# Kernel optimization log

Hardware: AMD Instinct MI355X
Metric: run time of the kernel (lower is better)

Reference implementation:

```python
import jax, jax.numpy as jnp
import numpy as np

H = 400      # LSTM hidden units
K = 10       # attention window mixture components (mixtures=30 -> alpha/beta/kappa of size K)
V = 61       # vocab_size
NOUT = 121   # MDN head: 1 eos + 20*(pi, mu1, mu2, sigma1, sigma2, rho)


def setup_inputs():
    key = jax.random.key(0)
    ks = jax.random.split(key, 12)
    B, T, U = 32, 600, 64
    s = 0.05
    d = {}
    d['strokes'] = jax.random.normal(ks[0], (B, T, 3), jnp.float32)
    d['sentence'] = jax.random.uniform(ks[1], (B, U, V), dtype=jnp.float32)
    d['W1'] = jax.random.normal(ks[2], (3 + V, 4 * H), jnp.float32) * s
    d['U1r'] = jax.random.normal(ks[3], (H, 4 * H), jnp.float32) * s
    d['b1'] = jnp.zeros((4 * H,), jnp.float32)
    d['Ww'] = jax.random.normal(ks[4], (H, 3 * K), jnp.float32) * s
    d['bw'] = jnp.zeros((3 * K,), jnp.float32)
    d['W2'] = jax.random.normal(ks[5], (3 + V + H, 4 * H), jnp.float32) * s
    d['U2r'] = jax.random.normal(ks[6], (H, 4 * H), jnp.float32) * s
    d['b2'] = jnp.zeros((4 * H,), jnp.float32)
    d['W3'] = jax.random.normal(ks[7], (3 + V + H, 4 * H), jnp.float32) * s
    d['U3r'] = jax.random.normal(ks[8], (H, 4 * H), jnp.float32) * s
    d['b3'] = jnp.zeros((4 * H,), jnp.float32)
    d['Wm'] = jax.random.normal(ks[9], (3 * H, NOUT), jnp.float32) * s
    d['bm'] = jnp.zeros((NOUT,), jnp.float32)
    return d


def _lstm(x_tbd, W, Ur, b, h0, c0):
    # standard Keras-order (i, f, g, o) LSTM over time-major input [T,B,D]
    def step(carry, xt):
        h, c = carry
        z = xt @ W + h @ Ur + b
        i, f, g, o = jnp.split(z, 4, axis=-1)
        c = jax.nn.sigmoid(f) * c + jax.nn.sigmoid(i) * jnp.tanh(g)
        h = jax.nn.sigmoid(o) * jnp.tanh(c)
        return (h, c), h
    _, hs = jax.lax.scan(step, (h0, c0), x_tbd)
    return hs


def _forward(strokes, sentence, W1, U1r, b1, Ww, bw, W2, U2r, b2, W3, U3r, b3, Wm, bm):
    B, T, _ = strokes.shape
    U = sentence.shape[1]
    u_grid = jnp.arange(U, dtype=strokes.dtype)           # character positions
    x_tb = jnp.transpose(strokes, (1, 0, 2))               # [T,B,3]
    h0 = jnp.zeros((B, H), strokes.dtype)
    w0 = jnp.zeros((B, V), strokes.dtype)
    k0 = jnp.zeros((B, K), strokes.dtype)

    def step1(carry, xt):
        # Graves synthesis windowed LSTM cell: LSTM on [x_t, w_{t-1}],
        # then Gaussian-mixture soft attention over the sentence.
        h, c, w, kappa = carry
        xin = jnp.concatenate([xt, w], axis=-1)            # [B, 3+V]
        z = xin @ W1 + h @ U1r + b1
        i, f, g, o = jnp.split(z, 4, axis=-1)
        c = jax.nn.sigmoid(f) * c + jax.nn.sigmoid(i) * jnp.tanh(g)
        h = jax.nn.sigmoid(o) * jnp.tanh(c)
        p = h @ Ww + bw                                    # [B, 3K]
        alpha = jnp.exp(p[:, :K])
        beta = jnp.exp(p[:, K:2 * K])
        kappa = kappa + jnp.exp(p[:, 2 * K:])
        # phi(u) = sum_k alpha_k exp(-beta_k (kappa_k - u)^2)  -> [B,U]
        phi = jnp.einsum('bk,bku->bu', alpha,
                         jnp.exp(-beta[:, :, None] * (kappa[:, :, None] - u_grid) ** 2))
        w = jnp.einsum('bu,buv->bv', phi, sentence)        # soft window [B,V]
        return (h, c, w, kappa), jnp.concatenate([h, w], axis=-1)

    _, o1 = jax.lax.scan(step1, (h0, h0, w0, k0), x_tb)    # [T,B,H+V]
    lstm1 = o1[:, :, :H]
    win = o1[:, :, H:]
    in2 = jnp.concatenate([x_tb, win, lstm1], axis=-1)     # skip1: [T,B,3+V+H]
    lstm2 = _lstm(in2, W2, U2r, b2, h0, h0)
    in3 = jnp.concatenate([x_tb, win, lstm2], axis=-1)     # skip2
    lstm3 = _lstm(in3, W3, U3r, b3, h0, h0)
    y = jnp.concatenate([lstm1, lstm2, lstm3], axis=-1) @ Wm + bm  # [T,B,121]
    # MDN mixture coefficients
    e = jax.nn.sigmoid(y[..., 0:1])
    pi = jax.nn.softmax(y[..., 1:21], axis=-1)
    mu1 = y[..., 21:41]
    mu2 = y[..., 41:61]
    s1 = jnp.exp(y[..., 61:81])
    s2 = jnp.exp(y[..., 81:101])
    rho = jnp.tanh(y[..., 101:121])
    out = jnp.concatenate([e, pi, mu1, mu2, s1, s2, rho], axis=-1)
    return jnp.transpose(out, (1, 0, 2))                   # [B,T,121]


def reference(strokes, sentence, W1, U1r, b1, Ww, bw, W2, U2r, b2, W3, U3r, b3, Wm, bm):
    return _forward(strokes, sentence, W1, U1r, b1, Ww, bw, W2, U2r, b2, W3, U3r, b3, Wm, bm)
```

## Files before the change

kernel.cpp:

```cpp
#include <hip/hip_runtime.h>
#include <math.h>

#define T 600
#define NBLK 235

#define FL1 256
#define FL2 768
#define FL3 1280
#define FLB 1792
#define SH1 2304
#define SH2 2880
#define SH3 3520

#define OFF_UT1 8192
#define SZ_UT1 (1600*480)
#define OFF_UT2 (OFF_UT1 + SZ_UT1)
#define SZ_UT2 (1600*960)
#define OFF_UT3 (OFF_UT2 + SZ_UT2)
#define OFF_WWT (OFF_UT3 + SZ_UT2)
#define SZ_WWT (30*400)
#define OFF_H1 (OFF_WWT + SZ_WWT)
#define SZ_H (600*32*400)
#define OFF_H2 (OFF_H1 + SZ_H)
#define OFF_H3 (OFF_H2 + SZ_H)
#define OFF_W  (OFF_H3 + SZ_H)
#define SZ_W (600*32*61)

#define LDS_W    0
#define LDS_V    19280
#define LDS_Z    34640
#define LDS_C    35408
#define LDS_TOT  35600

__device__ __forceinline__ float sigm(float x) { return 1.f/(1.f+expf(-x)); }

__global__ void init_ws(unsigned* uws) {
    for (int i = threadIdx.x + blockIdx.x*blockDim.x; i < 8192; i += blockDim.x*gridDim.x)
        uws[i] = 0u;
}

__global__ void build_ut(float* __restrict__ ws,
                         const float* __restrict__ W1, const float* __restrict__ U1r,
                         const float* __restrict__ W2, const float* __restrict__ U2r,
                         const float* __restrict__ W3, const float* __restrict__ U3r,
                         const float* __restrict__ Ww) {
    const long N1 = 1600L*480, N2 = 1600L*960;
    const long total = N1 + 2*N2 + 30L*400;
    for (long i = blockIdx.x*(long)blockDim.x + threadIdx.x; i < total;
         i += (long)gridDim.x*blockDim.x) {
        if (i < N1) {
            long c = i / 480, k = i % 480;
            float v = 0.f;
            if (k < 64) v = W1[k*1600 + c];
            else if (k < 464) v = U1r[(k-64)*1600 + c];
            ws[OFF_UT1 + c*480 + k] = v;
        } else if (i < N1 + N2) {
            long ii = i - N1; long c = ii/960, k = ii%960;
            float v = 0.f;
            if (k < 464) v = W2[k*1600 + c];
            else if (k >= 480 && k < 880) v = U2r[(k-480)*1600 + c];
            ws[OFF_UT2 + c*960 + k] = v;
        } else if (i < N1 + 2*N2) {
            long ii = i - N1 - N2; long c = ii/960, k = ii%960;
            float v = 0.f;
            if (k < 464) v = W3[k*1600 + c];
            else if (k >= 480 && k < 880) v = U3r[(k-480)*1600 + c];
            ws[OFF_UT3 + c*960 + k] = v;
        } else {
            long ii = i - N1 - 2*N2; long n = ii/400, k = ii%400;
            ws[OFF_WWT + n*400 + k] = Ww[k*30 + n];
        }
    }
}

__device__ __forceinline__ unsigned ld_cohere(const unsigned* p) {
    unsigned v;
    asm volatile("global_load_dword %0, %1, off sc0 sc1\n\t"
                 "s_waitcnt vmcnt(0)"
                 : "=v"(v) : "v"(p) : "memory");
    return v;
}
__device__ __forceinline__ void st_wt(float* p, float v) {
    asm volatile("global_store_dword %0, %1, off sc0 sc1\n\t"
                 "s_waitcnt vmcnt(0)"
                 :: "v"(p), "v"(v) : "memory");
}
__device__ __forceinline__ void publish(unsigned* flags, unsigned v) {
    #pragma unroll
    for (int r = 0; r < 8; ++r)
        asm volatile("global_store_dword %0, %1, off sc0 sc1"
                     :: "v"(flags + r*64), "v"(v) : "memory");
    asm volatile("s_waitcnt vmcnt(0)" ::: "memory");
}
__device__ __forceinline__ void wait_flag(const unsigned* p, unsigned tgt) {
    int it = 0;
    while (ld_cohere(p) < tgt) {
        if (it > 32) __builtin_amdgcn_s_sleep(2);
        ++it;
    }
}
__device__ __forceinline__ void arrive2(unsigned* shard, unsigned gsize,
                                        unsigned* master, unsigned n,
                                        unsigned* flags, unsigned ep1) {
    unsigned old = __hip_atomic_fetch_add(shard, 1u, __ATOMIC_RELAXED,
                                          __HIP_MEMORY_SCOPE_AGENT);
    if (old + 1u == gsize * ep1) {
        unsigned o2 = __hip_atomic_fetch_add(master, gsize, __ATOMIC_RELAXED,
                                             __HIP_MEMORY_SCOPE_AGENT);
        if (o2 + gsize == n * ep1) publish(flags, ep1);
    }
}
__device__ __forceinline__ void arrive1(unsigned* master, unsigned n,
                                        unsigned* flags, unsigned ep1) {
    unsigned old = __hip_atomic_fetch_add(master, 1u, __ATOMIC_RELAXED,
                                          __HIP_MEMORY_SCOPE_AGENT);
    if (old + 1u == n * ep1) publish(flags, ep1);
}

template<int NQ, int KCN, int K4S, int LO, int HI>
__device__ __forceinline__ void gemm_pass(const float4* __restrict__ w4,
                                          const float4* __restrict__ v4,
                                          int lc0, int kc, int bq, int kofs4,
                                          float acc[8][4]) {
    #pragma unroll
    for (int q = 0; q < NQ; ++q) {
        int kfv = q*KCN + kc;
        if (kfv >= LO && kfv < HI) {
            int xv = kfv ^ ((kfv >> 3) & 7);
            int kfw = kofs4 + kfv;
            int xw = kfw ^ ((kfw >> 3) & 7);
            float4 va[8];
            #pragma unroll
            for (int i = 0; i < 8; ++i) va[i] = v4[(bq*8+i)*120 + xv];
            #pragma unroll
            for (int j = 0; j < 4; ++j) {
                float4 u = w4[(lc0+j)*K4S + xw];
                #pragma unroll
                for (int i = 0; i < 8; ++i)
                    acc[i][j] += va[i].x*u.x + va[i].y*u.y + va[i].z*u.z + va[i].w*u.w;
            }
        }
    }
}

__launch_bounds__(512)
__global__ void hw_main(float* __restrict__ ws,
                        const float* __restrict__ strokes, const float* __restrict__ sentence,
                        const float* __restrict__ b1, const float* __restrict__ b2,
                        const float* __restrict__ b3, const float* __restrict__ bw) {
    extern __shared__ float S[];
    const int tid = threadIdx.x;
    const int bid = blockIdx.x;
    unsigned* uws = (unsigned*)ws;
    unsigned* root1 = uws + 0;
    unsigned* root2 = uws + 64;
    unsigned* root3 = uws + 128;
    unsigned* rootB = uws + 192;
    const int rep = (bid & 7) * 64;
    const unsigned* fl1r = uws + FL1 + rep;
    const unsigned* fl2r = uws + FL2 + rep;
    const unsigned* flBr = uws + FLB + rep;

    int role, unit0 = 0, nu = 0, L = 0, b0a = 0;
    const float* utp = nullptr; const float* biasp = nullptr; float* hout = nullptr;
    if (bid < 67)       { role = 0; L = bid;      unit0 = L*6; nu = (bid==66)?4:6; utp = ws+OFF_UT1; biasp = b1; hout = ws+OFF_H1; }
    else if (bid < 147) { role = 1; L = bid-67;   unit0 = L*5; nu = 5;             utp = ws+OFF_UT2; biasp = b2; hout = ws+OFF_H2; }
    else if (bid < 227) { role = 2; L = bid-147;  unit0 = L*5; nu = 5;             utp = ws+OFF_UT3; biasp = b3; hout = ws+OFF_H3; }
    else                { role = 3; b0a = (bid-227)*4; }

    if (role <= 2) {
        const int NC = 4*nu;
        const int KCN = (role == 0) ? 20 : 24;
        const int K4S = (role == 0) ? 121 : 241;
        const int K4TOT = (role == 0) ? 120 : 240;
        const int uts = (role == 0) ? 480 : 960;
        float4* w4 = (float4*)S;
        float4* v4 = (float4*)(S + LDS_V);
        float*  vf = S + LDS_V;
        float*  z_lds = S + LDS_Z;
        float*  c_lds = S + LDS_C;

        for (int idx = tid; idx < NC*K4TOT; idx += 512) {
            int colL = idx / K4TOT, kf = idx % K4TOT;
            int gcol = (colL/nu)*400 + unit0 + (colL%nu);
            float4 val = *(const float4*)(utp + (size_t)gcol*uts + kf*4);
            w4[colL*K4S + (kf ^ ((kf>>3)&7))] = val;
        }
        for (int i = tid; i < 192; i += 512) c_lds[i] = 0.f;

        const int tile = tid / KCN, kc = tid % KCN;
        const int bq = tile / nu, cq = tile % nu;
        const bool act = (tile < 4*nu);
        float bias0 = 0.f, bias1 = 0.f;
        if (tid < 32*NC)       { int lc = tid % NC;        bias0 = biasp[(lc/nu)*400 + unit0 + (lc%nu)]; }
        if (tid + 512 < 32*NC) { int lc = (tid+512) % NC;  bias1 = biasp[(lc/nu)*400 + unit0 + (lc%nu)]; }
        const unsigned nrole = (role == 0) ? 67u : 80u;
        unsigned* mymaster = (role == 0) ? root1 : ((role == 1) ? root2 : root3);
        unsigned* myfl     = uws + ((role == 0) ? FL1 : ((role == 1) ? FL2 : FL3));
        const unsigned* myflr = uws + ((role == 0) ? FL1 : ((role == 1) ? FL2 : FL3)) + rep;
        unsigned* myshard;
        {
            int shbase = (role == 0) ? SH1 : ((role == 1) ? SH2 : SH3);
            myshard = uws + shbase + (L >> 3) * 64;
        }
        const unsigned gsize = (unsigned)(((int)nrole - (L >> 3)*8 < 8) ? ((int)nrole - (L >> 3)*8) : 8);
        __syncthreads();

        for (int t = 0; t < T; ++t) {
            float acc[8][4];
            #pragma unroll
            for (int i = 0; i < 8; ++i)
                #pragma unroll
                for (int j = 0; j < 4; ++j) acc[i][j] = 0.f;

            if (role == 0) {
                if (tid == 0 && t > 0) wait_flag(myflr, (unsigned)t);
                __syncthreads();
                const float* hsrc = (t > 0) ? (ws + OFF_H1 + (size_t)(t-1)*12800) : nullptr;
                for (int idx = tid; idx < 32*104; idx += 512) {
                    int b = idx/104, kf = 16 + idx%104;
                    float4 val = {0.f,0.f,0.f,0.f};
                    if (kf < 116 && hsrc) val = *(const float4*)(hsrc + b*400 + (kf*4 - 64));
                    v4[b*120 + (kf ^ ((kf>>3)&7))] = val;
                }
                __syncthreads();
                if (act) gemm_pass<6,20,121,16,116>(w4, v4, cq*4, kc, bq, 0, acc);
                if (tid == 0 && t > 0) wait_flag(flBr, (unsigned)t);
                __syncthreads();
                const float* wsrc = (t > 0) ? (ws + OFF_W + (size_t)(t-1)*1952) : nullptr;
                {
                    int b = tid / 16, kf = tid % 16;
                    if (b < 32) {
                        float4 val;
                        if (kf == 0) {
                            const float* xp = strokes + ((size_t)b*600 + t)*3;
                            val.x = xp[0]; val.y = xp[1]; val.z = xp[2];
                            val.w = wsrc ? wsrc[b*61] : 0.f;
                        } else {
                            int k0 = kf*4 - 3;
                            if (wsrc) { val.x = wsrc[b*61+k0]; val.y = wsrc[b*61+k0+1];
                                        val.z = wsrc[b*61+k0+2]; val.w = wsrc[b*61+k0+3]; }
                            else { val.x=val.y=val.z=val.w=0.f; }
                        }
                        v4[b*120 + (kf ^ ((kf>>3)&7))] = val;
                    }
                }
                __syncthreads();
                if (act) gemm_pass<6,20,121,0,16>(w4, v4, cq*4, kc, bq, 0, acc);
            } else {
                if (tid == 0) wait_flag((role==1) ? fl1r : fl2r, (unsigned)(t+1));
                __syncthreads();
                const float* hsrc = ws + ((role==1)?OFF_H1:OFF_H2) + (size_t)t*12800;
                for (int idx = tid; idx < 32*104; idx += 512) {
                    int b = idx/104, kf = 16 + idx%104;
                    float4 val = {0.f,0.f,0.f,0.f};
                    if (kf < 116) val = *(const float4*)(hsrc + b*400 + (kf*4 - 64));
                    v4[b*120 + (kf ^ ((kf>>3)&7))] = val;
                }
                __syncthreads();
                if (act) gemm_pass<5,24,241,16,116>(w4, v4, cq*4, kc, bq, 0, acc);
                if (tid == 0) wait_flag(flBr, (unsigned)(t+1));
                __syncthreads();
                const float* wsrc = ws + OFF_W + (size_t)t*1952;
                {
                    int b = tid / 16, kf = tid % 16;
                    if (b < 32) {
                        float4 val;
                        if (kf == 0) {
                            const float* xp = strokes + ((size_t)b*600 + t)*3;
                            val.x = xp[0]; val.y = xp[1]; val.z = xp[2];
                            val.w = wsrc[b*61];
                        } else {
                            int k0 = kf*4 - 3;
                            val.x = wsrc[b*61+k0]; val.y = wsrc[b*61+k0+1];
                            val.z = wsrc[b*61+k0+2]; val.w = wsrc[b*61+k0+3];
                        }
                        v4[b*120 + (kf ^ ((kf>>3)&7))] = val;
                    }
                }
                __syncthreads();
                if (act) gemm_pass<5,24,241,0,16>(w4, v4, cq*4, kc, bq, 0, acc);
                __syncthreads();
                if (tid == 0 && t > 0) wait_flag(myflr, (unsigned)t);
                __syncthreads();
                const float* hp2 = (t > 0) ? (ws + ((role==1)?OFF_H2:OFF_H3) + (size_t)(t-1)*12800) : nullptr;
                for (int idx = tid; idx < 32*120; idx += 512) {
                    int b = idx/120, kf = idx%120;
                    float4 val = {0.f,0.f,0.f,0.f};
                    if (kf < 100 && hp2) val = *(const float4*)(hp2 + b*400 + kf*4);
                    v4[b*120 + (kf ^ ((kf>>3)&7))] = val;
                }
                __syncthreads();
                if (act) gemm_pass<5,24,241,0,100>(w4, v4, cq*4, kc, bq, 120, acc);
            }

            __syncthreads();
            const int halfk = (KCN+1)/2;
            const int SCRW = NC*32 + 4;
            const int NO = 32*NC;
            if (act && kc < halfk) {
                #pragma unroll
                for (int i = 0; i < 8; ++i) {
                    float4 w;
                    w.x=acc[i][0]; w.y=acc[i][1]; w.z=acc[i][2]; w.w=acc[i][3];
                    *(float4*)&vf[kc*SCRW + (bq*8+i)*NC + cq*4] = w;
                }
            }
            __syncthreads();
            float zs0 = 0.f, zs1 = 0.f;
            if (tid < NO)       for (int k2 = 0; k2 < halfk; ++k2) zs0 += vf[k2*SCRW + tid];
            if (tid + 512 < NO) for (int k2 = 0; k2 < halfk; ++k2) zs1 += vf[k2*SCRW + tid + 512];
            __syncthreads();
            if (act && kc >= halfk) {
                #pragma unroll
                for (int i = 0; i < 8; ++i) {
                    float4 w;
                    w.x=acc[i][0]; w.y=acc[i][1]; w.z=acc[i][2]; w.w=acc[i][3];
                    *(float4*)&vf[(kc-halfk)*SCRW + (bq*8+i)*NC + cq*4] = w;
                }
            }
            __syncthreads();
            const int rem = KCN - halfk;
            if (tid < NO) {
                for (int k2 = 0; k2 < rem; ++k2) zs0 += vf[k2*SCRW + tid];
                z_lds[tid] = zs0 + bias0;
            }
            if (tid + 512 < NO) {
                for (int k2 = 0; k2 < rem; ++k2) zs1 += vf[k2*SCRW + tid + 512];
                z_lds[tid + 512] = zs1 + bias1;
            }
            __syncthreads();
            if (tid < 32*nu) {
                int b = tid & 31, ju = tid >> 5;
                float zi = z_lds[b*NC + ju];
                float zf = z_lds[b*NC + nu + ju];
                float zg = z_lds[b*NC + 2*nu + ju];
                float zo = z_lds[b*NC + 3*nu + ju];
                float cP = c_lds[b*6 + ju];
                float cN = sigm(zf)*cP + sigm(zi)*tanhf(zg);
                float hN = sigm(zo)*tanhf(cN);
                c_lds[b*6 + ju] = cN;
                st_wt(&hout[(size_t)t*12800 + b*400 + unit0 + ju], hN);
            }
            __syncthreads();
            if (tid == 0) arrive2(myshard, gsize, mymaster, nrole, myfl, (unsigned)(t+1));
        }
    } else {
        float* hb   = S;
        float* pp   = S + 1600;
        float* pbuf = S + 2080;
        float* ab   = S + 2208;
        float* phiB = S + 2304;
        float* kap  = S + 2560;
        float* bwl  = S + 2600;
        float* sentl= S + 2640;
        float* wwt  = S + 18256;

        for (int i = tid; i < 40; i += 512) kap[i] = 0.f;
        for (int i = tid; i < 30; i += 512) bwl[i] = bw[i];
        for (int i = tid; i < 15616; i += 512) sentl[i] = sentence[(size_t)b0a*3904 + i];
        for (int i = tid; i < 12000; i += 512) {
            int n = i/400, k = i%400;
            wwt[n*401 + k] = ws[OFF_WWT + i];
        }
        __syncthreads();

        for (int t = 0; t < T; ++t) {
            if (tid == 0) wait_flag(fl1r, (unsigned)(t+1));
            __syncthreads();
            const float* h1t = ws + OFF_H1 + (size_t)t*12800 + (size_t)b0a*400;
            if (tid < 400) *(float4*)&hb[tid*4] = *(const float4*)(h1t + tid*4);
            __syncthreads();
            if (tid < 480) {
                int bb = tid/120, r = tid%120, n = r >> 2, kc4 = r & 3;
                const float* wwn = wwt + n*401;
                float sacc = 0.f;
                for (int k = kc4*100; k < kc4*100 + 100; ++k) sacc += hb[bb*400 + k]*wwn[k];
                pp[bb*120 + n*4 + kc4] = sacc;
            }
            __syncthreads();
            if (tid < 120) {
                int bb = tid/30, n = tid%30;
                pbuf[tid] = pp[bb*120+n*4] + pp[bb*120+n*4+1] + pp[bb*120+n*4+2] + pp[bb*120+n*4+3] + bwl[n];
            }
            __syncthreads();
            if (tid < 40) {
                int bb = tid/10, k0 = tid%10;
                float a  = expf(pbuf[bb*30 + k0]);
                float be = expf(pbuf[bb*30 + 10 + k0]);
                float kv = kap[bb*10 + k0] + expf(pbuf[bb*30 + 20 + k0]);
                kap[bb*10 + k0] = kv;
                ab[bb*20 + k0] = a;
                ab[bb*20 + 10 + k0] = be;
            }
            __syncthreads();
            if (tid < 256) {
                int bb = tid/64, u = tid%64;
                float uf = (float)u, ph = 0.f;
                for (int k0 = 0; k0 < 10; ++k0) {
                    float d = kap[bb*10 + k0] - uf;
                    ph += ab[bb*20 + k0]*expf(-ab[bb*20 + 10 + k0]*d*d);
                }
                phiB[tid] = ph;
            }
            __syncthreads();
            if (tid < 244) {
                int bb = tid/61, v = tid%61;
                const float* sp = sentl + bb*3904 + v;
                float wv = 0.f;
                for (int u = 0; u < 64; ++u) wv += phiB[bb*64 + u]*sp[u*61];
                st_wt(&ws[OFF_W + (size_t)t*1952 + (b0a+bb)*61 + v], wv);
            }
            __syncthreads();
            if (tid == 0) arrive1(rootB, 8u, uws + FLB, (unsigned)(t+1));
        }
    }
}

__launch_bounds__(256)
__global__ void out_proj(const float* __restrict__ ws, const float* __restrict__ Wm,
                         const float* __restrict__ bm, float* __restrict__ out) {
    __shared__ __align__(16) float hc[8*1200];
    __shared__ float yy[8*121];
    __shared__ float sm2[16];
    const int tid = threadIdx.x;
    const long rowbase = (long)blockIdx.x * 8;
    const float* h1h = ws + OFF_H1;
    const float* h2h = ws + OFF_H2;
    const float* h3h = ws + OFF_H3;
    for (int idx = tid; idx < 8*1200; idx += 256) {
        int i = idx/1200, k = idx%1200;
        long r = rowbase + i; int t = (int)(r >> 5), b = (int)(r & 31);
        float v;
        if (k < 400)      v = h1h[(size_t)t*12800 + b*400 + k];
        else if (k < 800) v = h2h[(size_t)t*12800 + b*400 + (k-400)];
        else              v = h3h[(size_t)t*12800 + b*400 + (k-800)];
        hc[i*1200 + k] = v;
    }
    __syncthreads();
    const int j = tid & 127, rr = tid >> 7;
    if (j < 121) {
        float a0=0.f, a1=0.f, a2=0.f, a3=0.f;
        const float* r0 = &hc[(rr*4+0)*1200];
        const float* r1 = &hc[(rr*4+1)*1200];
        const float* r2 = &hc[(rr*4+2)*1200];
        const float* r3 = &hc[(rr*4+3)*1200];
        for (int k = 0; k < 1200; ++k) {
            float wm = Wm[(size_t)k*121 + j];
            a0 += r0[k]*wm; a1 += r1[k]*wm; a2 += r2[k]*wm; a3 += r3[k]*wm;
        }
        float bb = bm[j];
        yy[(rr*4+0)*121 + j] = a0 + bb;
        yy[(rr*4+1)*121 + j] = a1 + bb;
        yy[(rr*4+2)*121 + j] = a2 + bb;
        yy[(rr*4+3)*121 + j] = a3 + bb;
    }
    __syncthreads();
    if (tid < 8) {
        const float* yr = &yy[tid*121];
        float m = yr[1];
        for (int q = 2; q < 21; ++q) m = fmaxf(m, yr[q]);
        float ssum = 0.f;
        for (int q = 1; q < 21; ++q) ssum += expf(yr[q] - m);
        sm2[tid*2] = m; sm2[tid*2+1] = ssum;
    }
    __syncthreads();
    if (j < 121) {
        for (int i2 = 0; i2 < 4; ++i2) {
            int i = rr*4 + i2;
            long r = rowbase + i; int t = (int)(r >> 5), b = (int)(r & 31);
            float y = yy[i*121 + j], o;
            if (j == 0)      o = 1.f/(1.f + expf(-y));
            else if (j < 21) o = expf(y - sm2[i*2]) / sm2[i*2+1];
            else if (j < 61) o = y;
            else if (j < 101) o = expf(y);
            else             o = tanhf(y);
            out[((size_t)b*600 + t)*121 + j] = o;
        }
    }
}

extern "C" void kernel_launch(void* const* d_in, const int* in_sizes, int n_in,
                              void* d_out, int out_size, void* d_ws, size_t ws_size,
                              hipStream_t stream) {
    const float* strokes  = (const float*)d_in[0];
    const float* sentence = (const float*)d_in[1];
    const float* W1  = (const float*)d_in[2];
    const float* U1r = (const float*)d_in[3];
    const float* b1  = (const float*)d_in[4];
    const float* Ww  = (const float*)d_in[5];
    const float* bw  = (const float*)d_in[6];
    const float* W2  = (const float*)d_in[7];
    const float* U2r = (const float*)d_in[8];
    const float* b2  = (const float*)d_in[9];
    const float* W3  = (const float*)d_in[10];
    const float* U3r = (const float*)d_in[11];
    const float* b3  = (const float*)d_in[12];
    const float* Wm  = (const float*)d_in[13];
    const float* bm  = (const float*)d_in[14];
    float* ws = (float*)d_ws;
    float* out = (float*)d_out;

    const int dyn_bytes = LDS_TOT * 4;
    (void)hipFuncSetAttribute((const void*)hw_main,
                              hipFuncAttributeMaxDynamicSharedMemorySize, dyn_bytes);

    init_ws<<<dim3(4), dim3(512), 0, stream>>>((unsigned*)ws);
    build_ut<<<dim3(1024), dim3(256), 0, stream>>>(ws, W1, U1r, W2, U2r, W3, U3r, Ww);
    hw_main<<<dim3(NBLK), dim3(512), dyn_bytes, stream>>>(ws, strokes, sentence, b1, b2, b3, bw);
    out_proj<<<dim3(2400), dim3(256), 0, stream>>>(ws, Wm, bm, out);
}
```

Measured before the change: 10.38 ms.

## Compute attention window redundantly in each layer-1 block to drop window flag wait

```diff
diff --git a/kernel.cpp b/kernel.cpp
--- a/kernel.cpp
+++ b/kernel.cpp
@@ -25,12 +25,19 @@
 #define OFF_H3 (OFF_H2 + SZ_H)
 #define OFF_W  (OFF_H3 + SZ_H)
 #define SZ_W (600*32*61)
+#define OFF_SP (OFF_W + SZ_W)
+#define SZ_SP (32*64*64)
 
 #define LDS_W    0
 #define LDS_V    19280
 #define LDS_Z    34640
 #define LDS_C    35408
 #define LDS_TOT  35600
+#define A0_KAP 11616
+#define A0_P   11936
+#define A0_AB  12896
+#define A0_PHI 13536
+#define A0_WB  15584
 
 __device__ __forceinline__ float sigm(float x) { return 1.f/(1.f+expf(-x)); }
 
@@ -43,9 +50,9 @@
                          const float* __restrict__ W1, const float* __restrict__ U1r,
                          const float* __restrict__ W2, const float* __restrict__ U2r,
                          const float* __restrict__ W3, const float* __restrict__ U3r,
-                         const float* __restrict__ Ww) {
+                         const float* __restrict__ Ww, const float* __restrict__ sentence) {
     const long N1 = 1600L*480, N2 = 1600L*960;
-    const long total = N1 + 2*N2 + 30L*400;
+    const long total = N1 + 2*N2 + 30L*400 + SZ_SP;
     for (long i = blockIdx.x*(long)blockDim.x + threadIdx.x; i < total;
          i += (long)gridDim.x*blockDim.x) {
         if (i < N1) {
@@ -66,9 +73,13 @@
             if (k < 464) v = W3[k*1600 + c];
             else if (k >= 480 && k < 880) v = U3r[(k-480)*1600 + c];
             ws[OFF_UT3 + c*960 + k] = v;
-        } else {
+        } else if (i < N1 + 2*N2 + 12000) {
             long ii = i - N1 - 2*N2; long n = ii/400, k = ii%400;
             ws[OFF_WWT + n*400 + k] = Ww[k*30 + n];
+        } else {
+            long ii = i - N1 - 2*N2 - 12000;
+            long b = ii >> 12, r = ii & 4095, u = r >> 6, v = r & 63;
+            ws[OFF_SP + ii] = (v < 61) ? sentence[b*3904 + u*61 + v] : 0.f;
         }
     }
 }
@@ -179,6 +190,11 @@
         float*  vf = S + LDS_V;
         float*  z_lds = S + LDS_Z;
         float*  c_lds = S + LDS_C;
+        float* kapL  = S + A0_KAP;
+        float* pbufL = S + A0_P;
+        float* abL   = S + A0_AB;
+        float* phiL  = S + A0_PHI;
+        float* wbufL = S + A0_WB;
 
         for (int idx = tid; idx < NC*K4TOT; idx += 512) {
             int colL = idx / K4TOT, kf = idx % K4TOT;
@@ -187,6 +203,10 @@
             w4[colL*K4S + (kf ^ ((kf>>3)&7))] = val;
         }
         for (int i = tid; i < 192; i += 512) c_lds[i] = 0.f;
+        if (role == 0) {
+            for (int i = tid; i < 320; i += 512) kapL[i] = 0.f;
+            for (int i = tid; i < 1952; i += 512) wbufL[i] = 0.f;
+        }
 
         const int tile = tid / KCN, kc = tid % KCN;
         const int bq = tile / nu, cq = tile % nu;
@@ -224,29 +244,87 @@
                     v4[b*120 + (kf ^ ((kf>>3)&7))] = val;
                 }
                 __syncthreads();
-                if (act) gemm_pass<6,20,121,16,116>(w4, v4, cq*4, kc, bq, 0, acc);
-                if (tid == 0 && t > 0) wait_flag(flBr, (unsigned)t);
-                __syncthreads();
-                const float* wsrc = (t > 0) ? (ws + OFF_W + (size_t)(t-1)*1952) : nullptr;
+                if (t > 0) {
+                    if (tid < 480) {
+                        int n = tid % 30, g = tid / 30;
+                        int bA = g*2, bB = bA + 1;
+                        const float4* wt4 = (const float4*)(ws + OFF_WWT) + n*100;
+                        float a0 = 0.f, a1 = 0.f;
+                        #pragma unroll 4
+                        for (int kfi = 0; kfi < 100; ++kfi) {
+                            int kf = kfi + 16;
+                            int xv = kf ^ ((kf>>3)&7);
+                            float4 wv = wt4[kfi];
+                            float4 hA = v4[bA*120 + xv];
+                            float4 hB = v4[bB*120 + xv];
+                            a0 += hA.x*wv.x + hA.y*wv.y + hA.z*wv.z + hA.w*wv.w;
+                            a1 += hB.x*wv.x + hB.y*wv.y + hB.z*wv.z + hB.w*wv.w;
+                        }
+                        float bwn = bw[n];
+                        pbufL[bA*30 + n] = a0 + bwn;
+                        pbufL[bB*30 + n] = a1 + bwn;
+                    }
+                    __syncthreads();
+                    if (tid < 320) {
+                        int b = tid/10, k0 = tid%10;
+                        float al = expf(pbufL[b*30 + k0]);
+                        float be = expf(pbufL[b*30 + 10 + k0]);
+                        kapL[b*10 + k0] += expf(pbufL[b*30 + 20 + k0]);
+                        abL[b*20 + k0] = al;
+                        abL[b*20 + 10 + k0] = be;
+                    }
+                    __syncthreads();
+                    for (int o = tid; o < 2048; o += 512) {
+                        int b = o >> 6, u = o & 63;
+                        float uf = (float)u, ph = 0.f;
+                        #pragma unroll
+                        for (int k0 = 0; k0 < 10; ++k0) {
+                            float d = kapL[b*10 + k0] - uf;
+                            ph += abL[b*20 + k0]*expf(-abL[b*20 + 10 + k0]*d*d);
+                        }
+                        phiL[o] = ph;
+                    }
+                    __syncthreads();
+                    {
+                        int b = tid >> 4, v4i = tid & 15;
+                        const float4* sp4 = (const float4*)(ws + OFF_SP) + ((size_t)b*64)*16 + v4i;
+                        const float* phb = phiL + b*64;
+                        float4 a4 = {0.f,0.f,0.f,0.f};
+                        #pragma unroll 4
+                        for (int u = 0; u < 64; ++u) {
+                            float pv = phb[u];
+                            float4 s4 = sp4[(size_t)u*16];
+                            a4.x += pv*s4.x; a4.y += pv*s4.y;
+                            a4.z += pv*s4.z; a4.w += pv*s4.w;
+                        }
+                        int v0 = v4i*4;
+                        wbufL[b*61 + v0] = a4.x;
+                        if (v0 + 3 < 61) {
+                            wbufL[b*61 + v0+1] = a4.y;
+                            wbufL[b*61 + v0+2] = a4.z;
+                            wbufL[b*61 + v0+3] = a4.w;
+                        }
+                    }
+                    __syncthreads();
+                }
                 {
-                    int b = tid / 16, kf = tid % 16;
+                    int b = tid >> 4, kf = tid & 15;
                     if (b < 32) {
                         float4 val;
                         if (kf == 0) {
                             const float* xp = strokes + ((size_t)b*600 + t)*3;
                             val.x = xp[0]; val.y = xp[1]; val.z = xp[2];
-                            val.w = wsrc ? wsrc[b*61] : 0.f;
+                            val.w = wbufL[b*61];
                         } else {
                             int k0 = kf*4 - 3;
-                            if (wsrc) { val.x = wsrc[b*61+k0]; val.y = wsrc[b*61+k0+1];
-                                        val.z = wsrc[b*61+k0+2]; val.w = wsrc[b*61+k0+3]; }
-                            else { val.x=val.y=val.z=val.w=0.f; }
+                            val.x = wbufL[b*61+k0];   val.y = wbufL[b*61+k0+1];
+                            val.z = wbufL[b*61+k0+2]; val.w = wbufL[b*61+k0+3];
                         }
                         v4[b*120 + (kf ^ ((kf>>3)&7))] = val;
                     }
                 }
                 __syncthreads();
-                if (act) gemm_pass<6,20,121,0,16>(w4, v4, cq*4, kc, bq, 0, acc);
+                if (act) gemm_pass<6,20,121,0,116>(w4, v4, cq*4, kc, bq, 0, acc);
             } else {
                 if (tid == 0) wait_flag((role==1) ? fl1r : fl2r, (unsigned)(t+1));
                 __syncthreads();
@@ -506,7 +584,7 @@
                               hipFuncAttributeMaxDynamicSharedMemorySize, dyn_bytes);
 
     init_ws<<<dim3(4), dim3(512), 0, stream>>>((unsigned*)ws);
-    build_ut<<<dim3(1024), dim3(256), 0, stream>>>(ws, W1, U1r, W2, U2r, W3, U3r, Ww);
+    build_ut<<<dim3(1024), dim3(256), 0, stream>>>(ws, W1, U1r, W2, U2r, W3, U3r, Ww, sentence);
     hw_main<<<dim3(NBLK), dim3(512), dyn_bytes, stream>>>(ws, strokes, sentence, b1, b2, b3, bw);
     out_proj<<<dim3(2400), dim3(256), 0, stream>>>(ws, Wm, bm, out);
 }
```

Measured after the change: 27.85 ms. 2.68x slower.

## Restructure attention window block to one wavefront per batch row

Applied to the files above, without the earlier changes.

```diff
diff --git a/kernel.cpp b/kernel.cpp
--- a/kernel.cpp
+++ b/kernel.cpp
@@ -33,6 +33,11 @@
 #define LDS_TOT  35600
 
 __device__ __forceinline__ float sigm(float x) { return 1.f/(1.f+expf(-x)); }
+
+#define WBAR() do { \
+    asm volatile("s_waitcnt lgkmcnt(0)" ::: "memory"); \
+    __builtin_amdgcn_sched_barrier(0); \
+} while (0)
 
 __global__ void init_ws(unsigned* uws) {
     for (int i = threadIdx.x + blockIdx.x*blockDim.x; i < 8192; i += blockDim.x*gridDim.x)
@@ -95,7 +100,7 @@
 __device__ __forceinline__ void wait_flag(const unsigned* p, unsigned tgt) {
     int it = 0;
     while (ld_cohere(p) < tgt) {
-        if (it > 32) __builtin_amdgcn_s_sleep(2);
+        if (it > 64) __builtin_amdgcn_s_sleep(2);
         ++it;
     }
 }
@@ -346,70 +351,76 @@
             if (tid == 0) arrive2(myshard, gsize, mymaster, nrole, myfl, (unsigned)(t+1));
         }
     } else {
+        const int wv = tid >> 6, lane = tid & 63;
         float* hb   = S;
-        float* pp   = S + 1600;
-        float* pbuf = S + 2080;
-        float* ab   = S + 2208;
-        float* phiB = S + 2304;
-        float* kap  = S + 2560;
-        float* bwl  = S + 2600;
-        float* sentl= S + 2640;
-        float* wwt  = S + 18256;
-
-        for (int i = tid; i < 40; i += 512) kap[i] = 0.f;
-        for (int i = tid; i < 30; i += 512) bwl[i] = bw[i];
+        float* pb   = S + 1600 + (tid>>6)*32;
+        float* ab   = S + 1792 + (tid>>6)*32;
+        float* kap  = S + 1984 + (tid>>6)*16;
+        float* phiW = S + 2112 + (tid>>6)*64;
+        float* sentl= S + 2368;
+        float* wwt  = S + 2368 + 15616;
+        float* hbW  = hb + wv*400;
+        float4* hb4 = (float4*)hbW;
+
+        for (int i = tid; i < 64; i += 512) (S + 1984)[i] = 0.f;
         for (int i = tid; i < 15616; i += 512) sentl[i] = sentence[(size_t)b0a*3904 + i];
         for (int i = tid; i < 12000; i += 512) {
             int n = i/400, k = i%400;
-            wwt[n*401 + k] = ws[OFF_WWT + i];
-        }
+            wwt[n*404 + k] = ws[OFF_WWT + i];
+        }
+        float bwv = (lane < 60 && !(lane & 1)) ? bw[lane >> 1] : 0.f;
         __syncthreads();
 
         for (int t = 0; t < T; ++t) {
-            if (tid == 0) wait_flag(fl1r, (unsigned)(t+1));
-            __syncthreads();
-            const float* h1t = ws + OFF_H1 + (size_t)t*12800 + (size_t)b0a*400;
-            if (tid < 400) *(float4*)&hb[tid*4] = *(const float4*)(h1t + tid*4);
-            __syncthreads();
-            if (tid < 480) {
-                int bb = tid/120, r = tid%120, n = r >> 2, kc4 = r & 3;
-                const float* wwn = wwt + n*401;
-                float sacc = 0.f;
-                for (int k = kc4*100; k < kc4*100 + 100; ++k) sacc += hb[bb*400 + k]*wwn[k];
-                pp[bb*120 + n*4 + kc4] = sacc;
-            }
-            __syncthreads();
-            if (tid < 120) {
-                int bb = tid/30, n = tid%30;
-                pbuf[tid] = pp[bb*120+n*4] + pp[bb*120+n*4+1] + pp[bb*120+n*4+2] + pp[bb*120+n*4+3] + bwl[n];
-            }
-            __syncthreads();
-            if (tid < 40) {
-                int bb = tid/10, k0 = tid%10;
-                float a  = expf(pbuf[bb*30 + k0]);
-                float be = expf(pbuf[bb*30 + 10 + k0]);
-                float kv = kap[bb*10 + k0] + expf(pbuf[bb*30 + 20 + k0]);
-                kap[bb*10 + k0] = kv;
-                ab[bb*20 + k0] = a;
-                ab[bb*20 + 10 + k0] = be;
-            }
-            __syncthreads();
-            if (tid < 256) {
-                int bb = tid/64, u = tid%64;
-                float uf = (float)u, ph = 0.f;
-                for (int k0 = 0; k0 < 10; ++k0) {
-                    float d = kap[bb*10 + k0] - uf;
-                    ph += ab[bb*20 + k0]*expf(-ab[bb*20 + 10 + k0]*d*d);
-                }
-                phiB[tid] = ph;
-            }
-            __syncthreads();
-            if (tid < 244) {
-                int bb = tid/61, v = tid%61;
-                const float* sp = sentl + bb*3904 + v;
-                float wv = 0.f;
-                for (int u = 0; u < 64; ++u) wv += phiB[bb*64 + u]*sp[u*61];
-                st_wt(&ws[OFF_W + (size_t)t*1952 + (b0a+bb)*61 + v], wv);
+            if (wv < 4) {
+                {
+                    int it = 0;
+                    while (ld_cohere(fl1r) < (unsigned)(t+1)) {
+                        if (it > 64) __builtin_amdgcn_s_sleep(2);
+                        ++it;
+                    }
+                }
+                const float* h1t = ws + OFF_H1 + (size_t)t*12800 + (size_t)(b0a+wv)*400;
+                for (int i = lane; i < 100; i += 64)
+                    hb4[i] = *(const float4*)(h1t + i*4);
+                WBAR();
+                if (lane < 60) {
+                    int n = lane >> 1, hf = lane & 1;
+                    const float4* ww4 = (const float4*)(wwt + n*404) + hf*50;
+                    const float4* hh4 = hb4 + hf*50;
+                    float a = 0.f;
+                    #pragma unroll 5
+                    for (int i = 0; i < 50; ++i) {
+                        float4 h = hh4[i], w = ww4[i];
+                        a += h.x*w.x + h.y*w.y + h.z*w.z + h.w*w.w;
+                    }
+                    a += __shfl_xor(a, 1);
+                    if (hf == 0) pb[n] = a + bwv;
+                }
+                WBAR();
+                if (lane < 10) {
+                    ab[lane]      = expf(pb[lane]);
+                    ab[16 + lane] = expf(pb[10 + lane]);
+                    kap[lane]    += expf(pb[20 + lane]);
+                }
+                WBAR();
+                {
+                    float uf = (float)lane, ph = 0.f;
+                    #pragma unroll
+                    for (int k0 = 0; k0 < 10; ++k0) {
+                        float d = kap[k0] - uf;
+                        ph += ab[k0]*expf(-ab[16 + k0]*d*d);
+                    }
+                    phiW[lane] = ph;
+                }
+                WBAR();
+                if (lane < 61) {
+                    const float* sp = sentl + wv*3904 + lane;
+                    float wvv = 0.f;
+                    #pragma unroll 4
+                    for (int u = 0; u < 64; ++u) wvv += phiW[u]*sp[u*61];
+                    st_wt(&ws[OFF_W + (size_t)t*1952 + (size_t)(b0a+wv)*61 + lane], wvv);
+                }
             }
             __syncthreads();
             if (tid == 0) arrive1(rootB, 8u, uws + FLB, (unsigned)(t+1));
```

Result: no change. 10.35 ms (-0.4%).
